# Kernel tuning notes

Measured on AMD Instinct MI355X. Metric: run time of the kernel, lower is better.

The kernel has to match this reference:

```python
import jax, jax.numpy as jnp
import numpy as np

B, D_MODEL, HIDEEN, HEAD, IMG_H, IMG_W = 16, 512, 512, 8, 32, 32
D_K = D_MODEL // HEAD
EPS = 1e-5


def setup_inputs() -> dict:
    key = jax.random.key(0)
    ks = jax.random.split(key, 9)
    s_in = 1.0 / np.sqrt(D_MODEL)
    s_h = 1.0 / np.sqrt(HIDEEN)
    return {
        "x": jax.random.normal(ks[0], (B, D_MODEL, IMG_H, IMG_W), jnp.float32),
        "Wq": jax.random.uniform(ks[1], (HIDEEN, D_MODEL), jnp.float32, -s_in, s_in),
        "bq": jax.random.uniform(ks[2], (HIDEEN,), jnp.float32, -s_in, s_in),
        "Wk": jax.random.uniform(ks[3], (HIDEEN, D_MODEL), jnp.float32, -s_in, s_in),
        "bk": jax.random.uniform(ks[4], (HIDEEN,), jnp.float32, -s_in, s_in),
        "Wv": jax.random.uniform(ks[5], (HIDEEN, D_MODEL), jnp.float32, -s_in, s_in),
        "bv": jax.random.uniform(ks[6], (HIDEEN,), jnp.float32, -s_in, s_in),
        "Wo": jax.random.uniform(ks[7], (HIDEEN, HIDEEN), jnp.float32, -s_h, s_h),
        "bo": jax.random.uniform(ks[8], (HIDEEN,), jnp.float32, -s_h, s_h),
    }


def _conv1x1(x, W, b):
    # x: [B, Cin, H, W], W: [Cout, Cin]
    return jnp.einsum("bchw,oc->bohw", x, W) + b[None, :, None, None]


def _heads(t):
    # torch: [B, C, H, W] -> view(B, -1, head, d_k) -> transpose(1, 2)
    return t.reshape(B, -1, HEAD, D_K).transpose(0, 2, 1, 3)  # [B, head, N, d_k]


def reference(x, Wq, bq, Wk, bk, Wv, bv, Wo, bo):
    q = _heads(_conv1x1(x, Wq, bq))
    k = _heads(_conv1x1(x, Wk, bk))
    v = _heads(_conv1x1(x, Wv, bv))
    scores = jnp.einsum("bhnd,bhmd->bhnm", q, k) / np.sqrt(D_K).astype(np.float32)
    attn = jax.nn.softmax(scores, axis=-1)
    out = jnp.einsum("bhnm,bhmd->bhnd", attn, v)  # [B, head, N, d_k]
    # back to image layout: [B, N, head*d_k] -> [B, hideen, H, W]
    out = out.transpose(0, 2, 1, 3).reshape(B, -1, HEAD * D_K)
    out = out.transpose(0, 2, 1).reshape(B, -1, IMG_H, IMG_W)
    out = _conv1x1(out, Wo, bo)
    # InstanceNorm2d (affine=False, biased var, eps=1e-5)
    mu = out.mean(axis=(2, 3), keepdims=True)
    var = out.var(axis=(2, 3), keepdims=True)
    out = (out - mu) / jnp.sqrt(var + EPS)
    # original applies the SAME attn_out conv a second time
    out = _conv1x1(out, Wo, bo)
    return out
```

## Files before the change

kernel.cpp:

```cpp
#include <hip/hip_runtime.h>


typedef short bf16x8_t __attribute__((ext_vector_type(8)));
typedef float f32x4_t  __attribute__((ext_vector_type(4)));

union U4 {
  uint4 u;
  bf16x8_t v;
  unsigned short us[8];
};

__device__ __forceinline__ unsigned short f2bf(float f) {
  union { float f; unsigned int u; } x; x.f = f;
  unsigned int r = x.u + 0x7fffu + ((x.u >> 16) & 1u);
  return (unsigned short)(r >> 16);
}

#define AS1 __attribute__((address_space(1)))
#define AS3 __attribute__((address_space(3)))

__device__ __forceinline__ void gload16(const unsigned short* g,
                                        unsigned short* l) {
  __builtin_amdgcn_global_load_lds((const AS1 unsigned int*)g,
                                   (AS3 unsigned int*)l, 16, 0, 0);
}

#define BATCH_STRIDE (512 * 1024)

__global__ __launch_bounds__(256) void cvtx_k(
    const float* __restrict__ x, unsigned short* __restrict__ xb)
{
  __shared__ float tile[32][33];
  const int b = blockIdx.z, c0 = blockIdx.y * 32, n0 = blockIdx.x * 32;
  const int t = threadIdx.x;
  {
    const int cl_ = t >> 3, n4 = (t & 7) * 4;
    const float4 u = *(const float4*)(x + (size_t)b * BATCH_STRIDE
                                      + (size_t)(c0 + cl_) * 1024 + n0 + n4);
    tile[cl_][n4] = u.x; tile[cl_][n4 + 1] = u.y;
    tile[cl_][n4 + 2] = u.z; tile[cl_][n4 + 3] = u.w;
  }
  __syncthreads();
  {
    const int nl = t >> 3, c4 = (t & 7) * 4;
    ushort4 o;
    o.x = f2bf(tile[c4][nl]);     o.y = f2bf(tile[c4 + 1][nl]);
    o.z = f2bf(tile[c4 + 2][nl]); o.w = f2bf(tile[c4 + 3][nl]);
    *(ushort4*)(xb + (size_t)b * BATCH_STRIDE + (size_t)(n0 + nl) * 512
                + c0 + c4) = o;
  }
}

__global__ __launch_bounds__(256) void cvtw_k(
    const float* __restrict__ s0, const float* __restrict__ s1,
    const float* __restrict__ s2, unsigned short* __restrict__ dst)
{
  const float* s = (blockIdx.y == 0) ? s0 : (blockIdx.y == 1) ? s1 : s2;
  const int i = (blockIdx.x * 256 + threadIdx.x) * 8;
  const float4 a = *(const float4*)(s + i);
  const float4 c = *(const float4*)(s + i + 4);
  U4 o;
  o.us[0] = f2bf(a.x); o.us[1] = f2bf(a.y);
  o.us[2] = f2bf(a.z); o.us[3] = f2bf(a.w);
  o.us[4] = f2bf(c.x); o.us[5] = f2bf(c.y);
  o.us[6] = f2bf(c.z); o.us[7] = f2bf(c.w);
  *(uint4*)(dst + (size_t)blockIdx.y * 262144 + i) = o.u;
}

template<int OUTF>
__device__ __forceinline__ void gemm_core(
    const unsigned short* __restrict__ Wb, const float* __restrict__ bias,
    const unsigned short* __restrict__ src, void* __restrict__ dst,
    int m0, int n0, int b, float scale,
    unsigned short* sA, unsigned short* sB)
{
  const int t = threadIdx.x;
  const int lane = t & 63, wv = t >> 6, qd = lane >> 4, cl = lane & 15;
  const int wm = wv >> 1, wn = wv & 1;
  const unsigned short* srcb = src + (size_t)b * BATCH_STRIDE + (size_t)n0 * 512;
  const unsigned short* wrow = Wb + (size_t)m0 * 512;

  const int lr = lane >> 2, ls = (lane & 3) * 8;
  const int r0 = wv * 32;

  f32x4_t acc[4][4];
  #pragma unroll
  for (int i = 0; i < 4; ++i)
    #pragma unroll
    for (int f = 0; f < 4; ++f) acc[i][f] = (f32x4_t){0.f, 0.f, 0.f, 0.f};

  for (int kk = 0; kk < 512; kk += 32) {
    if (kk) __syncthreads();
    gload16(wrow + (size_t)(r0 + lr) * 512 + kk + ls,      sA + r0 * 32);
    gload16(wrow + (size_t)(r0 + 16 + lr) * 512 + kk + ls, sA + (r0 + 16) * 32);
    gload16(srcb + (size_t)(r0 + lr) * 512 + kk + ls,      sB + r0 * 32);
    gload16(srcb + (size_t)(r0 + 16 + lr) * 512 + kk + ls, sB + (r0 + 16) * 32);
    __syncthreads();

    U4 af[4], bf[4];
    #pragma unroll
    for (int i = 0; i < 4; ++i) {
      af[i].u = *(const uint4*)(sA + (wm * 64 + i * 16 + cl) * 32 + qd * 8);
      bf[i].u = *(const uint4*)(sB + (wn * 64 + i * 16 + cl) * 32 + qd * 8);
    }
    #pragma unroll
    for (int i = 0; i < 4; ++i)
      #pragma unroll
      for (int f = 0; f < 4; ++f)
        acc[i][f] = __builtin_amdgcn_mfma_f32_16x16x32_bf16(
            af[i].v, bf[f].v, acc[i][f], 0, 0, 0);
  }

  #pragma unroll
  for (int i = 0; i < 4; ++i) {
    #pragma unroll
    for (int r = 0; r < 4; ++r) {
      const int o = m0 + wm * 64 + i * 16 + qd * 4 + r;
      const float bv = bias[o];
      #pragma unroll
      for (int f = 0; f < 4; ++f) {
        const int n = n0 + wn * 64 + f * 16 + cl;
        const size_t idx = (size_t)b * BATCH_STRIDE + (size_t)o * 1024 + n;
        const float val = (acc[i][f][r] + bv) * scale;
        if (OUTF) ((float*)dst)[idx] = val;
        else      ((unsigned short*)dst)[idx] = f2bf(val);
      }
    }
  }
}

struct QKVArgs {
  const unsigned short* W[3];
  const float* bias[3];
  unsigned short* dst[3];
  float scale[3];
};

__global__ __launch_bounds__(256) void qkv_k(
    QKVArgs args, const unsigned short* __restrict__ xb)
{
  __shared__ __align__(16) unsigned short sA[128 * 32];
  __shared__ __align__(16) unsigned short sB[128 * 32];
  const int widx = blockIdx.y >> 2;
  const int m0 = (blockIdx.y & 3) * 128;
  gemm_core<0>(args.W[widx], args.bias[widx], xb, args.dst[widx],
               m0, blockIdx.x * 128, blockIdx.z, args.scale[widx], sA, sB);
}

template<int OUTF>
__global__ __launch_bounds__(256) void gemm_wo_k(
    const unsigned short* __restrict__ Wb, const float* __restrict__ bias,
    const unsigned short* __restrict__ src, void* __restrict__ dst)
{
  __shared__ __align__(16) unsigned short sA[128 * 32];
  __shared__ __align__(16) unsigned short sB[128 * 32];
  gemm_core<OUTF>(Wb, bias, src, dst, blockIdx.y * 128, blockIdx.x * 128,
                  blockIdx.z, 1.0f, sA, sB);
}

__global__ __launch_bounds__(256) void vt_k(
    const unsigned short* __restrict__ src, unsigned short* __restrict__ dst)
{
  __shared__ unsigned short tile[32][36];
  const int b = blockIdx.z, j0 = blockIdx.y * 32, p0 = blockIdx.x * 32;
  const int t = threadIdx.x;
  {
    const int pr = t >> 3, jc = (t & 7) * 4;
    *(ushort4*)&tile[pr][jc] = *(const ushort4*)(
        src + (size_t)b * BATCH_STRIDE + (size_t)(p0 + pr) * 512 + j0 + jc);
  }
  __syncthreads();
  {
    const int jr = t >> 3, pc = (t & 7) * 4;
    ushort4 o;
    o.x = tile[pc][jr];     o.y = tile[pc + 1][jr];
    o.z = tile[pc + 2][jr]; o.w = tile[pc + 3][jr];
    *(ushort4*)(dst + (size_t)b * BATCH_STRIDE + (size_t)(j0 + jr) * 1024
                + p0 + pc) = o;
  }
}

__global__ __launch_bounds__(256) void attn_k(
    const unsigned short* __restrict__ Q,
    const unsigned short* __restrict__ K,
    const unsigned short* __restrict__ Vt,
    unsigned short* __restrict__ O)
{
  __shared__ __align__(16) unsigned short sK[64 * 64];
  __shared__ __align__(16) unsigned short sV[64 * 64];
  __shared__ __align__(16) unsigned short sP[4 * 16 * 72];

  const int t = threadIdx.x;
  const int lane = t & 63, wv = t >> 6, qd = lane >> 4, cl = lane & 15;

  const int g = blockIdx.y * 16 + blockIdx.x;
  const int xcd = g & 7, rest = g >> 3;
  const int iblk = rest & 15;
  const int bh = (rest >> 4) * 8 + xcd;
  const int b = bh >> 3, h = bh & 7;
  const int i0 = iblk * 64;
  const size_t bbase = (size_t)b * BATCH_STRIDE;
  const int hoff = h * 64;

  U4 aq0, aq1;
  {
    const unsigned short* qp =
        Q + bbase + (size_t)(i0 + wv * 16 + cl) * 512 + hoff + qd * 8;
    aq0.u = *(const uint4*)qp;
    aq1.u = *(const uint4*)(qp + 32);
  }

  const int lrow = lane >> 3;
  const int lchk = ((lane & 7) ^ lrow) * 8;
  const int sw = cl & 7;
  const int c0r = (qd ^ sw) * 8;
  const int c1r = ((qd + 4) ^ sw) * 8;

  f32x4_t oacc[4];
  #pragma unroll
  for (int f = 0; f < 4; ++f) oacc[f] = (f32x4_t){0.f, 0.f, 0.f, 0.f};
  float rs[4] = {0.f, 0.f, 0.f, 0.f};

  #pragma unroll
  for (int p = 0; p < 2; ++p) {
    const int r = wv * 16 + p * 8;
    gload16(K + bbase + (size_t)(r + lrow) * 512 + hoff + lchk, sK + r * 64);
    gload16(Vt + bbase + (size_t)(hoff + r + lrow) * 1024 + lchk, sV + r * 64);
  }
  __syncthreads();

  for (int tt = 0; tt < 16; ++tt) {
    f32x4_t s[4];
    __builtin_amdgcn_s_setprio(1);
    #pragma unroll
    for (int nh = 0; nh < 4; ++nh) {
      s[nh] = (f32x4_t){0.f, 0.f, 0.f, 0.f};
      U4 bk0; bk0.u = *(const uint4*)(sK + (nh * 16 + cl) * 64 + c0r);
      U4 bk1; bk1.u = *(const uint4*)(sK + (nh * 16 + cl) * 64 + c1r);
      s[nh] = __builtin_amdgcn_mfma_f32_16x16x32_bf16(aq0.v, bk0.v, s[nh], 0, 0, 0);
      s[nh] = __builtin_amdgcn_mfma_f32_16x16x32_bf16(aq1.v, bk1.v, s[nh], 0, 0, 0);
    }
    __builtin_amdgcn_s_setprio(0);

    __syncthreads();
    if (tt < 15) {
      const int jn = (tt + 1) * 64;
      #pragma unroll
      for (int p = 0; p < 2; ++p) {
        const int r = wv * 16 + p * 8;
        gload16(K + bbase + (size_t)(jn + r + lrow) * 512 + hoff + lchk,
                sK + r * 64);
      }
    }

    #pragma unroll
    for (int nh = 0; nh < 4; ++nh) {
      #pragma unroll
      for (int r = 0; r < 4; ++r) {
        const float pv = __expf(s[nh][r]);
        sP[wv * 1152 + (qd * 4 + r) * 72 + nh * 16 + cl] = f2bf(pv);
        rs[r] += pv;
      }
    }

    asm volatile("s_waitcnt lgkmcnt(0)" ::: "memory");
    __builtin_amdgcn_sched_barrier(0);

    U4 pf0, pf1;
    pf0.u = *(const uint4*)(sP + wv * 1152 + cl * 72 + qd * 8);
    pf1.u = *(const uint4*)(sP + wv * 1152 + cl * 72 + 32 + qd * 8);
    __builtin_amdgcn_s_setprio(1);
    #pragma unroll
    for (int f = 0; f < 4; ++f) {
      U4 vf0, vf1;
      vf0.u = *(const uint4*)(sV + (f * 16 + cl) * 64 + c0r);
      vf1.u = *(const uint4*)(sV + (f * 16 + cl) * 64 + c1r);
      oacc[f] = __builtin_amdgcn_mfma_f32_16x16x32_bf16(pf0.v, vf0.v, oacc[f], 0, 0, 0);
      oacc[f] = __builtin_amdgcn_mfma_f32_16x16x32_bf16(pf1.v, vf1.v, oacc[f], 0, 0, 0);
    }
    __builtin_amdgcn_s_setprio(0);

    __syncthreads();
    if (tt < 15) {
      const int jn = (tt + 1) * 64;
      #pragma unroll
      for (int p = 0; p < 2; ++p) {
        const int r = wv * 16 + p * 8;
        gload16(Vt + bbase + (size_t)(hoff + r + lrow) * 1024 + jn + lchk,
                sV + r * 64);
      }
    }
  }

  #pragma unroll
  for (int m = 1; m < 16; m <<= 1)
    #pragma unroll
    for (int r = 0; r < 4; ++r) rs[r] += __shfl_xor(rs[r], m);

  #pragma unroll
  for (int f = 0; f < 4; ++f) {
    #pragma unroll
    for (int r = 0; r < 4; ++r) {
      const int i = i0 + wv * 16 + qd * 4 + r;
      const int j = hoff + f * 16 + cl;
      O[bbase + (size_t)i * 512 + j] = f2bf(oacc[f][r] / rs[r]);
    }
  }
}

__global__ __launch_bounds__(256) void norm_k(
    const float* __restrict__ x, unsigned short* __restrict__ y)
{
  __shared__ float tile[8][1028];
  __shared__ float shm[8], shv[8];
  const int b = blockIdx.x >> 6, c0 = (blockIdx.x & 63) * 8;
  const int t = threadIdx.x;
  const int ch = t >> 5, ln = t & 31;
  const float* xr = x + (size_t)b * BATCH_STRIDE + (size_t)(c0 + ch) * 1024;
  float s1 = 0.f, s2 = 0.f;
  #pragma unroll
  for (int j = 0; j < 8; ++j) {
    const int n = ln * 4 + j * 128;
    const float4 u = *(const float4*)(xr + n);
    tile[ch][n] = u.x; tile[ch][n + 1] = u.y;
    tile[ch][n + 2] = u.z; tile[ch][n + 3] = u.w;
    s1 += u.x + u.y + u.z + u.w;
    s2 += u.x * u.x + u.y * u.y + u.z * u.z + u.w * u.w;
  }
  #pragma unroll
  for (int m = 1; m < 32; m <<= 1) {
    s1 += __shfl_xor(s1, m);
    s2 += __shfl_xor(s2, m);
  }
  if (ln == 0) {
    const float mean = s1 * (1.f / 1024.f);
    const float var = s2 * (1.f / 1024.f) - mean * mean;
    shm[ch] = mean;
    shv[ch] = rsqrtf(var + 1e-5f);
  }
  __syncthreads();
  unsigned short* yb = y + (size_t)b * BATCH_STRIDE;
  #pragma unroll
  for (int jn = 0; jn < 4; ++jn) {
    const int n = t + jn * 256;
    U4 o;
    #pragma unroll
    for (int c = 0; c < 8; ++c)
      o.us[c] = f2bf((tile[c][n] - shm[c]) * shv[c]);
    *(uint4*)(yb + (size_t)n * 512 + c0) = o.u;
  }
}

extern "C" void kernel_launch(void* const* d_in, const int* in_sizes, int n_in,
                              void* d_out, int out_size, void* d_ws, size_t ws_size,
                              hipStream_t stream) {
  const float* x  = (const float*)d_in[0];
  const float* Wq = (const float*)d_in[1];
  const float* bq = (const float*)d_in[2];
  const float* Wk = (const float*)d_in[3];
  const float* bk = (const float*)d_in[4];
  const float* Wv = (const float*)d_in[5];
  const float* bv = (const float*)d_in[6];
  const float* Wo = (const float*)d_in[7];
  const float* bo = (const float*)d_in[8];

  const size_t BUF = (size_t)16 * BATCH_STRIDE;
  unsigned short* xb = (unsigned short*)d_ws;
  unsigned short* Qb = xb + BUF;
  unsigned short* Kb = Qb + BUF;
  unsigned short* Vb = (unsigned short*)d_out;
  unsigned short* Ob = Vb + BUF;
  unsigned short* Vt = xb;
  float*          out1f = (float*)d_ws;
  unsigned short* out1n = Kb;

  unsigned short* Wbf3 = Ob;
  unsigned short* WoA  = Vb;
  unsigned short* WoB  = xb;

  QKVArgs qa;
  qa.W[0] = Wbf3; qa.W[1] = Wbf3 + 262144; qa.W[2] = Wbf3 + 524288;
  qa.bias[0] = bq; qa.bias[1] = bk; qa.bias[2] = bv;
  qa.dst[0] = Qb; qa.dst[1] = Kb; qa.dst[2] = Vb;
  qa.scale[0] = 0.125f; qa.scale[1] = 1.0f; qa.scale[2] = 1.0f;

  cvtx_k<<<dim3(32, 16, 16), 256, 0, stream>>>(x, xb);
  cvtw_k<<<dim3(128, 3), 256, 0, stream>>>(Wq, Wk, Wv, Wbf3);
  qkv_k<<<dim3(8, 12, 16), 256, 0, stream>>>(qa, xb);
  vt_k<<<dim3(32, 16, 16), 256, 0, stream>>>(Vb, Vt);
  cvtw_k<<<dim3(128, 1), 256, 0, stream>>>(Wo, Wo, Wo, WoA);
  attn_k<<<dim3(16, 128), 256, 0, stream>>>(Qb, Kb, Vt, Ob);
  gemm_wo_k<1><<<dim3(8, 4, 16), 256, 0, stream>>>(WoA, bo, Ob, out1f);
  norm_k<<<dim3(16 * 64), 256, 0, stream>>>(out1f, out1n);
  cvtw_k<<<dim3(128, 1), 256, 0, stream>>>(Wo, Wo, Wo, WoB);
  gemm_wo_k<1><<<dim3(8, 4, 16), 256, 0, stream>>>(WoB, bo, out1n, d_out);
}
```

Before: 257.6 us.

## Process two 64-row query blocks per attention workgroup to reuse K/V tiles

Each attention workgroup now handles 128 query rows (two 64-row sub-blocks per wave) instead of 64, halving the grid. Every K and V tile loaded into shared memory is reused across both sub-blocks, which halves global K/V traffic and barrier count per query row. In exchange, register pressure rises from the doubled accumulators and score arrays, the grid shrinks to 1024 workgroups so occupancy and wave balance may drop, and the per-wave P buffer is reused serially between the two sub-blocks.

```diff
diff --git a/kernel.cpp b/kernel.cpp
--- a/kernel.cpp
+++ b/kernel.cpp
@@ -193,21 +193,22 @@
   const int t = threadIdx.x;
   const int lane = t & 63, wv = t >> 6, qd = lane >> 4, cl = lane & 15;
 
-  const int g = blockIdx.y * 16 + blockIdx.x;
+  const int g = blockIdx.y * 8 + blockIdx.x;
   const int xcd = g & 7, rest = g >> 3;
-  const int iblk = rest & 15;
-  const int bh = (rest >> 4) * 8 + xcd;
+  const int iblk = rest & 7;
+  const int bh = (rest >> 3) * 8 + xcd;
   const int b = bh >> 3, h = bh & 7;
-  const int i0 = iblk * 64;
+  const int i0 = iblk * 128;
   const size_t bbase = (size_t)b * BATCH_STRIDE;
   const int hoff = h * 64;
 
-  U4 aq0, aq1;
-  {
+  U4 aq[2][2];
+  #pragma unroll
+  for (int qb = 0; qb < 2; ++qb) {
     const unsigned short* qp =
-        Q + bbase + (size_t)(i0 + wv * 16 + cl) * 512 + hoff + qd * 8;
-    aq0.u = *(const uint4*)qp;
-    aq1.u = *(const uint4*)(qp + 32);
+        Q + bbase + (size_t)(i0 + qb * 64 + wv * 16 + cl) * 512 + hoff + qd * 8;
+    aq[qb][0].u = *(const uint4*)qp;
+    aq[qb][1].u = *(const uint4*)(qp + 32);
   }
 
   const int lrow = lane >> 3;
@@ -216,10 +217,14 @@
   const int c0r = (qd ^ sw) * 8;
   const int c1r = ((qd + 4) ^ sw) * 8;
 
-  f32x4_t oacc[4];
-  #pragma unroll
-  for (int f = 0; f < 4; ++f) oacc[f] = (f32x4_t){0.f, 0.f, 0.f, 0.f};
-  float rs[4] = {0.f, 0.f, 0.f, 0.f};
+  f32x4_t oacc[2][4];
+  #pragma unroll
+  for (int qb = 0; qb < 2; ++qb)
+    #pragma unroll
+    for (int f = 0; f < 4; ++f) oacc[qb][f] = (f32x4_t){0.f, 0.f, 0.f, 0.f};
+  float rs[2][4] = {{0.f, 0.f, 0.f, 0.f}, {0.f, 0.f, 0.f, 0.f}};
+
+  unsigned short* sPw = sP + wv * 1152;
 
   #pragma unroll
   for (int p = 0; p < 2; ++p) {
@@ -230,15 +235,19 @@
   __syncthreads();
 
   for (int tt = 0; tt < 16; ++tt) {
-    f32x4_t s[4];
+    f32x4_t s[2][4];
     __builtin_amdgcn_s_setprio(1);
     #pragma unroll
     for (int nh = 0; nh < 4; ++nh) {
-      s[nh] = (f32x4_t){0.f, 0.f, 0.f, 0.f};
       U4 bk0; bk0.u = *(const uint4*)(sK + (nh * 16 + cl) * 64 + c0r);
       U4 bk1; bk1.u = *(const uint4*)(sK + (nh * 16 + cl) * 64 + c1r);
-      s[nh] = __builtin_amdgcn_mfma_f32_16x16x32_bf16(aq0.v, bk0.v, s[nh], 0, 0, 0);
-      s[nh] = __builtin_amdgcn_mfma_f32_16x16x32_bf16(aq1.v, bk1.v, s[nh], 0, 0, 0);
+      #pragma unroll
+      for (int qb = 0; qb < 2; ++qb) {
+        f32x4_t z = (f32x4_t){0.f, 0.f, 0.f, 0.f};
+        z = __builtin_amdgcn_mfma_f32_16x16x32_bf16(aq[qb][0].v, bk0.v, z, 0, 0, 0);
+        z = __builtin_amdgcn_mfma_f32_16x16x32_bf16(aq[qb][1].v, bk1.v, z, 0, 0, 0);
+        s[qb][nh] = z;
+      }
     }
     __builtin_amdgcn_s_setprio(0);
 
@@ -254,31 +263,36 @@
     }
 
     #pragma unroll
-    for (int nh = 0; nh < 4; ++nh) {
-      #pragma unroll
-      for (int r = 0; r < 4; ++r) {
-        const float pv = __expf(s[nh][r]);
-        sP[wv * 1152 + (qd * 4 + r) * 72 + nh * 16 + cl] = f2bf(pv);
-        rs[r] += pv;
-      }
-    }
-
-    asm volatile("s_waitcnt lgkmcnt(0)" ::: "memory");
-    __builtin_amdgcn_sched_barrier(0);
-
-    U4 pf0, pf1;
-    pf0.u = *(const uint4*)(sP + wv * 1152 + cl * 72 + qd * 8);
-    pf1.u = *(const uint4*)(sP + wv * 1152 + cl * 72 + 32 + qd * 8);
-    __builtin_amdgcn_s_setprio(1);
-    #pragma unroll
-    for (int f = 0; f < 4; ++f) {
-      U4 vf0, vf1;
-      vf0.u = *(const uint4*)(sV + (f * 16 + cl) * 64 + c0r);
-      vf1.u = *(const uint4*)(sV + (f * 16 + cl) * 64 + c1r);
-      oacc[f] = __builtin_amdgcn_mfma_f32_16x16x32_bf16(pf0.v, vf0.v, oacc[f], 0, 0, 0);
-      oacc[f] = __builtin_amdgcn_mfma_f32_16x16x32_bf16(pf1.v, vf1.v, oacc[f], 0, 0, 0);
-    }
-    __builtin_amdgcn_s_setprio(0);
+    for (int qb = 0; qb < 2; ++qb) {
+      #pragma unroll
+      for (int nh = 0; nh < 4; ++nh) {
+        #pragma unroll
+        for (int r = 0; r < 4; ++r) {
+          const float pv = __expf(s[qb][nh][r]);
+          sPw[(qd * 4 + r) * 72 + nh * 16 + cl] = f2bf(pv);
+          rs[qb][r] += pv;
+        }
+      }
+
+      asm volatile("s_waitcnt lgkmcnt(0)" ::: "memory");
+      __builtin_amdgcn_sched_barrier(0);
+
+      U4 pf0, pf1;
+      pf0.u = *(const uint4*)(sPw + cl * 72 + qd * 8);
+      pf1.u = *(const uint4*)(sPw + cl * 72 + 32 + qd * 8);
+      __builtin_amdgcn_s_setprio(1);
+      #pragma unroll
+      for (int f = 0; f < 4; ++f) {
+        U4 vf0, vf1;
+        vf0.u = *(const uint4*)(sV + (f * 16 + cl) * 64 + c0r);
+        vf1.u = *(const uint4*)(sV + (f * 16 + cl) * 64 + c1r);
+        oacc[qb][f] = __builtin_amdgcn_mfma_f32_16x16x32_bf16(
+            pf0.v, vf0.v, oacc[qb][f], 0, 0, 0);
+        oacc[qb][f] = __builtin_amdgcn_mfma_f32_16x16x32_bf16(
+            pf1.v, vf1.v, oacc[qb][f], 0, 0, 0);
+      }
+      __builtin_amdgcn_s_setprio(0);
+    }
 
     __syncthreads();
     if (tt < 15) {
@@ -293,17 +307,20 @@
   }
 
   #pragma unroll
-  for (int m = 1; m < 16; m <<= 1)
-    #pragma unroll
-    for (int r = 0; r < 4; ++r) rs[r] += __shfl_xor(rs[r], m);
-
-  #pragma unroll
-  for (int f = 0; f < 4; ++f) {
-    #pragma unroll
-    for (int r = 0; r < 4; ++r) {
-      const int i = i0 + wv * 16 + qd * 4 + r;
-      const int j = hoff + f * 16 + cl;
-      O[bbase + (size_t)i * 512 + j] = f2bf(oacc[f][r] / rs[r]);
+  for (int qb = 0; qb < 2; ++qb) {
+    #pragma unroll
+    for (int m = 1; m < 16; m <<= 1)
+      #pragma unroll
+      for (int r = 0; r < 4; ++r) rs[qb][r] += __shfl_xor(rs[qb][r], m);
+
+    #pragma unroll
+    for (int f = 0; f < 4; ++f) {
+      #pragma unroll
+      for (int r = 0; r < 4; ++r) {
+        const int i = i0 + qb * 64 + wv * 16 + qd * 4 + r;
+        const int j = hoff + f * 16 + cl;
+        O[bbase + (size_t)i * 512 + j] = f2bf(oacc[qb][f][r] / rs[qb][r]);
+      }
     }
   }
 }
@@ -389,7 +406,7 @@
   qkv_k<<<dim3(8, 12, 16), 256, 0, stream>>>(qa, xb);
   vt_k<<<dim3(32, 16, 16), 256, 0, stream>>>(Vb, Vt);
   cvtw_k<<<dim3(128, 1), 256, 0, stream>>>(Wo, Wo, Wo, WoA);
-  attn_k<<<dim3(16, 128), 256, 0, stream>>>(Qb, Kb, Vt, Ob);
+  attn_k<<<dim3(8, 128), 256, 0, stream>>>(Qb, Kb, Vt, Ob);
   gemm_wo_k<1><<<dim3(8, 4, 16), 256, 0, stream>>>(WoA, bo, Ob, out1f);
   norm_k<<<dim3(16 * 64), 256, 0, stream>>>(out1f, out1n);
   cvtw_k<<<dim3(128, 1), 256, 0, stream>>>(Wo, Wo, Wo, WoB);
```

Measured after the change: 265.1 us. +2.9%, slower.
